# Optimization experiments

Measured on AMD Instinct MI355X. Metric: run time of the kernel, lower is better.

## Reference

```python
import jax, jax.numpy as jnp
import numpy as np

B_SZ, L_SEQ = 8, 4096
D_MODEL, D_CONV, D_MAMBA = 512, 256, 256
DSTATE, N_HEADS, K, FFN = 64, 4, 3, 2048
EPS = 1e-6


def setup_inputs() -> dict:
    key = jax.random.key(0)
    ks = jax.random.split(key, 14)
    def rn(k, shape, scale=0.02):
        return jax.random.normal(k, shape, jnp.float32) * scale
    return {
        "x": rn(ks[0], (B_SZ, L_SEQ, D_MODEL), 1.0),
        "velocity": rn(ks[1], (B_SZ, L_SEQ, D_MODEL), 0.1),
        "pre_norm_w": jnp.ones((D_MODEL,), jnp.float32),
        "conv_in_w": rn(ks[2], (D_MODEL, 2 * D_CONV)),
        "conv_dw_w": rn(ks[3], (D_CONV, K), 0.1),
        "conv_dw_b": jnp.zeros((D_CONV,), jnp.float32),
        "x_proj_w": rn(ks[4], (D_MODEL, D_MAMBA)),
        "dt_w": rn(ks[5], (D_MODEL, D_MAMBA), 0.001),
        "dt_b": jnp.full((D_MAMBA,), -4.0, jnp.float32),
        "B_w": rn(ks[6], (D_MODEL, DSTATE)),
        "C_w": rn(ks[7], (D_MODEL, DSTATE)),
        "A_log": jnp.tile(jnp.log(jnp.arange(1, DSTATE + 1, dtype=jnp.float32))[None, :], (N_HEADS, 1)),
        "D": jnp.ones((D_MAMBA,), jnp.float32),
        "ssm_out_w": rn(ks[8], (D_MAMBA, D_MAMBA)),
        "out_proj_w": rn(ks[9], (D_MODEL, D_MODEL)),
        "log_beta": jnp.asarray(0.0, jnp.float32),  # sigmoid(0)=0.5 = beta_init
        "ffn_norm_w": jnp.ones((D_MODEL,), jnp.float32),
        "w1": rn(ks[10], (D_MODEL, FFN)),
        "w3": rn(ks[11], (D_MODEL, FFN)),
        "w2": rn(ks[12], (FFN, D_MODEL)),
    }


def _rmsnorm(x, w):
    xf = x.astype(jnp.float32)
    r = jax.lax.rsqrt(jnp.mean(xf * xf, axis=-1, keepdims=True) + EPS)
    return (xf * r).astype(x.dtype) * w


def _gated_conv(xn, conv_in_w, conv_dw_w, conv_dw_b):
    # project to 2*d_conv, causal depthwise conv on first half, silu-gate with second half
    uv = xn @ conv_in_w                       # [B,L,2*dc]
    u, g = uv[..., :D_CONV], uv[..., D_CONV:]
    up = jnp.pad(u, ((0, 0), (K - 1, 0), (0, 0)))
    L = xn.shape[1]
    conv = conv_dw_b
    for k in range(K):                        # tiny fixed kernel loop
        conv = conv + up[:, k:k + L, :] * conv_dw_w[:, k]
    return conv * jax.nn.silu(g)              # [B,L,d_conv]


def _ssm(xn, x_proj_w, dt_w, dt_b, B_w, C_w, A_log, D, ssm_out_w):
    x_ssm = xn @ x_proj_w                                     # [B,L,dm]
    dt_raw = jnp.clip(xn @ dt_w + dt_b, -10.0, 5.0)
    dt = jnp.clip(jax.nn.softplus(dt_raw), 1e-4, 0.1)         # [B,L,dm]
    Bm = xn @ B_w                                             # [B,L,ds]
    Cm = xn @ C_w
    Bm = Bm / jnp.clip(jnp.linalg.norm(Bm, axis=-1, keepdims=True), 1.0)
    Cm = Cm / jnp.clip(jnp.linalg.norm(Cm, axis=-1, keepdims=True), 1.0)
    A = -jnp.exp(A_log.reshape(-1))                           # [dm], channel c -> head c//ds, state c%ds
    Bfull = jnp.tile(Bm, (1, 1, N_HEADS))                     # [B,L,dm]: B[..., c % ds]
    Cfull = jnp.tile(Cm, (1, 1, N_HEADS))
    decay = jnp.exp(dt * A)                                   # [B,L,dm]
    inp = dt * Bfull * x_ssm

    def step(h, di):
        d_, i_ = di
        h = d_ * h + i_
        return h, h

    h0 = jnp.zeros((xn.shape[0], D_MAMBA), x_ssm.dtype)
    _, hs = jax.lax.scan(step, h0, (jnp.swapaxes(decay, 0, 1), jnp.swapaxes(inp, 0, 1)))
    y = jnp.swapaxes(hs, 0, 1) * Cfull + D * x_ssm            # [B,L,dm]
    return y @ ssm_out_w


def reference(x, velocity, pre_norm_w, conv_in_w, conv_dw_w, conv_dw_b,
              x_proj_w, dt_w, dt_b, B_w, C_w, A_log, D, ssm_out_w,
              out_proj_w, log_beta, ffn_norm_w, w1, w3, w2):
    xn = _rmsnorm(x, pre_norm_w)
    conv_out = _gated_conv(xn, conv_in_w, conv_dw_w, conv_dw_b)
    ssm_out = _ssm(xn, x_proj_w, dt_w, dt_b, B_w, C_w, A_log, D, ssm_out_w)
    mixer = jnp.concatenate([conv_out, ssm_out], axis=-1) @ out_proj_w
    beta = jax.nn.sigmoid(log_beta)
    velocity = beta * velocity + mixer
    x = x + velocity
    # fused manual RMSNorm (fp32) + SwiGLU + residual
    xf = x.astype(jnp.float32)
    rms = jax.lax.rsqrt(jnp.mean(xf * xf, axis=-1, keepdims=True) + EPS)
    normed = (xf * rms).astype(x.dtype) * ffn_norm_w
    ffn = (jax.nn.silu(normed @ w1) * (normed @ w3)) @ w2
    x = x + ffn
    return (x, velocity)
```

## Files before the change

kernel.cpp:

```cpp
#include <hip/hip_runtime.h>

#define MTOK   32768
#define LSEQ   4096
#define BSZ    8
#define DM     512
#define DC     256
#define DMAMBA 256
#define DST    64
#define NPROJ  1152
#define FFN_D  2048
#define NCH    64
#define CLEN   64

typedef __attribute__((ext_vector_type(4))) float          f32x4;
typedef __attribute__((ext_vector_type(8))) unsigned short u16x8;
typedef __attribute__((ext_vector_type(8))) __bf16         bf16x8;

typedef const __attribute__((address_space(1))) unsigned int* gptr_t;
typedef __attribute__((address_space(3))) unsigned int*       lptr_t;

static __device__ __forceinline__ unsigned short f2bf(float f) {
    unsigned int u = __builtin_bit_cast(unsigned int, f);
    u += 0x7fffu + ((u >> 16) & 1u);
    return (unsigned short)(u >> 16);
}

static __device__ __forceinline__ float wred(float s) {
#pragma unroll
    for (int m = 1; m < 64; m <<= 1) s += __shfl_xor(s, m);
    return s;
}

static __device__ __forceinline__ f32x4 mfma16(u16x8 a, u16x8 b, f32x4 c) {
    return __builtin_amdgcn_mfma_f32_16x16x32_bf16(
        __builtin_bit_cast(bf16x8, a), __builtin_bit_cast(bf16x8, b), c, 0, 0, 0);
}

static __device__ __forceinline__ void gl16(const unsigned short* g, unsigned short* l) {
    __builtin_amdgcn_global_load_lds((gptr_t)g, (lptr_t)l, 16, 0, 0);
}

template <int EPI>
__global__ __launch_bounds__(256) void gemm_nt(
    const unsigned short* __restrict__ A, const unsigned short* __restrict__ Bt,
    const unsigned short* __restrict__ B2t, void* __restrict__ Cp,
    const float* __restrict__ Cin, int K, int ldc)
{
    __shared__ unsigned short As[128 * 32];
    __shared__ unsigned short Bs[128 * 32];
    __shared__ unsigned short Bs2[(EPI == 2) ? 128 * 32 : 8];

    const int tid = threadIdx.x;
    const int lane = tid & 63, wid = tid >> 6;
    const int wr = wid >> 1, wc = wid & 1;
    const long n0 = (long)blockIdx.x * 128;
    const long m0 = (long)blockIdx.y * 128;

    f32x4 acc[4][4], acc2[4][4];
#pragma unroll
    for (int i = 0; i < 4; i++)
#pragma unroll
        for (int j = 0; j < 4; j++) {
            acc[i][j] = f32x4{0.f, 0.f, 0.f, 0.f};
            acc2[i][j] = f32x4{0.f, 0.f, 0.f, 0.f};
        }

    const int srow = wid * 32 + (lane >> 2);
    const int scol = (lane & 3) * 8;
    const unsigned short* agp = A + (m0 + srow) * (long)K + scol;
    const unsigned short* bgp = Bt + (n0 + srow) * (long)K + scol;
    const unsigned short* b2gp = (EPI == 2) ? (B2t + (n0 + srow) * (long)K + scol) : nullptr;
    unsigned short* lA = As + wid * 1024;
    unsigned short* lB = Bs + wid * 1024;
    unsigned short* lB2 = (EPI == 2) ? (Bs2 + wid * 1024) : nullptr;

    const int fr = lane & 15, fo = (lane >> 4) * 8;
    const long skip = 16 * (long)K;

    for (int k0 = 0; k0 < K; k0 += 32) {
        gl16(agp + k0, lA);
        gl16(agp + k0 + skip, lA + 512);
        gl16(bgp + k0, lB);
        gl16(bgp + k0 + skip, lB + 512);
        if constexpr (EPI == 2) {
            gl16(b2gp + k0, lB2);
            gl16(b2gp + k0 + skip, lB2 + 512);
        }
        __syncthreads();

        u16x8 av[4], bv[4], cv[4];
#pragma unroll
        for (int i = 0; i < 4; i++)
            av[i] = *(const u16x8*)(As + (wr * 64 + i * 16 + fr) * 32 + fo);
#pragma unroll
        for (int j = 0; j < 4; j++)
            bv[j] = *(const u16x8*)(Bs + (wc * 64 + j * 16 + fr) * 32 + fo);
        if constexpr (EPI == 2) {
#pragma unroll
            for (int j = 0; j < 4; j++)
                cv[j] = *(const u16x8*)(Bs2 + (wc * 64 + j * 16 + fr) * 32 + fo);
        }
#pragma unroll
        for (int i = 0; i < 4; i++)
#pragma unroll
            for (int j = 0; j < 4; j++) {
                acc[i][j] = mfma16(av[i], bv[j], acc[i][j]);
                if constexpr (EPI == 2) acc2[i][j] = mfma16(av[i], cv[j], acc2[i][j]);
            }
        __syncthreads();
    }

    const int frow = (lane >> 4) * 4;
#pragma unroll
    for (int i = 0; i < 4; i++)
#pragma unroll
        for (int j = 0; j < 4; j++)
#pragma unroll
            for (int r = 0; r < 4; r++) {
                long row = m0 + wr * 64 + i * 16 + frow + r;
                long col = n0 + wc * 64 + j * 16 + fr;
                long idx = row * (long)ldc + col;
                float v = acc[i][j][r];
                if constexpr (EPI == 0) {
                    ((float*)Cp)[idx] = v;
                } else if constexpr (EPI == 1) {
                    ((unsigned short*)Cp)[idx] = f2bf(v);
                } else if constexpr (EPI == 2) {
                    float h3 = acc2[i][j][r];
                    float s = v / (1.f + __expf(-v));
                    ((unsigned short*)Cp)[idx] = f2bf(s * h3);
                } else {
                    ((float*)Cp)[idx] = Cin[idx] + v;
                }
            }
}

struct TD { const float* s; unsigned short* d; int K, N, nb; };
struct TP { TD t[10]; };

__global__ __launch_bounds__(256) void transpose_all_k(TP p)
{
    int b = blockIdx.x;
#pragma unroll
    for (int i = 0; i < 10; i++) {
        TD td = p.t[i];
        if (b < td.nb) {
            int idx = b * 256 + threadIdx.x;
            if (idx < td.K * td.N) {
                int k = idx / td.N, n = idx - k * td.N;
                td.d[(long)n * td.K + k] = f2bf(td.s[idx]);
            }
            return;
        }
        b -= td.nb;
    }
}

__global__ __launch_bounds__(256) void rmsnorm1_k(const float* __restrict__ x,
                                                  const float* __restrict__ w,
                                                  unsigned short* __restrict__ out)
{
    const int lane = threadIdx.x & 63, wv = threadIdx.x >> 6;
    const long tok = (long)blockIdx.x * 4 + wv;
    const float* xr = x + tok * DM;
    float4 v[2];
    float s = 0.f;
#pragma unroll
    for (int j = 0; j < 2; j++) {
        int d0 = j * 256 + lane * 4;
        v[j] = *(const float4*)(xr + d0);
        s += v[j].x * v[j].x + v[j].y * v[j].y + v[j].z * v[j].z + v[j].w * v[j].w;
    }
    s = wred(s);
    float r = rsqrtf(s * (1.f / DM) + 1e-6f);
#pragma unroll
    for (int j = 0; j < 2; j++) {
        int d0 = j * 256 + lane * 4;
        const float4 ww = *(const float4*)(w + d0);
        *(ushort4*)(out + tok * DM + d0) = make_ushort4(
            f2bf(v[j].x * r * ww.x), f2bf(v[j].y * r * ww.y),
            f2bf(v[j].z * r * ww.z), f2bf(v[j].w * r * ww.w));
    }
}

__global__ __launch_bounds__(256) void mamba_prep_k(
    const float* __restrict__ proj, const float* __restrict__ dt_b,
    const float* __restrict__ A_log, const float* __restrict__ conv_w,
    const float* __restrict__ conv_b,
    float* __restrict__ decay, float* __restrict__ inp, float* __restrict__ cmn,
    unsigned short* __restrict__ mixin)
{
    const int lane = threadIdx.x & 63, wv = threadIdx.x >> 6;
    const long tok = (long)blockIdx.x * 4 + wv;
    const int l = (int)(tok & (LSEQ - 1));
    const float* pr = proj + tok * NPROJ;

    float bv = pr[1024 + lane];
    float cv = pr[1088 + lane];
    float nb2 = wred(bv * bv);
    float nc2 = wred(cv * cv);
    float rb = 1.f / fmaxf(sqrtf(nb2), 1.f);
    float rc = 1.f / fmaxf(sqrtf(nc2), 1.f);
    float bn = bv * rb;
    cmn[tok * DST + lane] = cv * rc;

#pragma unroll
    for (int j = 0; j < 4; j++) {
        int d = j * 64 + lane;
        float dtr = pr[768 + d] + dt_b[d];
        dtr = fminf(fmaxf(dtr, -10.f), 5.f);
        float sp = log1pf(__expf(dtr));
        float dt = fminf(fmaxf(sp, 1e-4f), 0.1f);
        float a = -__expf(A_log[d]);
        decay[tok * DMAMBA + d] = __expf(dt * a);
        inp[tok * DMAMBA + d] = dt * bn * pr[512 + d];

        float ul  = pr[d];
        float um1 = (l >= 1) ? pr[d - NPROJ] : 0.f;
        float um2 = (l >= 2) ? pr[d - 2 * NPROJ] : 0.f;
        float conv = conv_b[d] + um2 * conv_w[d * 3] + um1 * conv_w[d * 3 + 1] + ul * conv_w[d * 3 + 2];
        float g = pr[256 + d];
        float sg = g / (1.f + __expf(-g));
        mixin[tok * DM + d] = f2bf(conv * sg);
    }
}

__global__ __launch_bounds__(256) void scan_chunk_k(const float* __restrict__ decay,
                                                    const float* __restrict__ inp,
                                                    float* __restrict__ P, float* __restrict__ S)
{
    const int bc = blockIdx.x;
    const int b = bc >> 6, c = bc & 63;
    const int d = threadIdx.x;
    long base = ((long)b * LSEQ + (long)c * CLEN) * DMAMBA + d;
    float h = 0.f, p = 1.f;
    for (int t = 0; t < CLEN; t++) {
        float dec = decay[base + (long)t * DMAMBA];
        float iv = inp[base + (long)t * DMAMBA];
        h = dec * h + iv;
        p *= dec;
    }
    P[(long)bc * DMAMBA + d] = p;
    S[(long)bc * DMAMBA + d] = h;
}

__global__ __launch_bounds__(256) void scan_prefix_k(const float* __restrict__ P,
                                                     const float* __restrict__ S,
                                                     float* __restrict__ carry)
{
    const int b = blockIdx.x, d = threadIdx.x;
    float H = 0.f;
    for (int c = 0; c < NCH; c++) {
        long i = ((long)b * NCH + c) * DMAMBA + d;
        carry[i] = H;
        H = P[i] * H + S[i];
    }
}

__global__ __launch_bounds__(256) void scan_finish_k(
    const float* __restrict__ decay, const float* __restrict__ inp,
    const float* __restrict__ carry, const float* __restrict__ cmn,
    const float* __restrict__ Dw, const float* __restrict__ proj,
    unsigned short* __restrict__ y)
{
    const int bc = blockIdx.x;
    const int b = bc >> 6, c = bc & 63;
    const int d = threadIdx.x;
    const long tok0 = (long)b * LSEQ + (long)c * CLEN;
    float h = carry[(long)bc * DMAMBA + d];
    const float dv = Dw[d];
    for (int t = 0; t < CLEN; t++) {
        long tok = tok0 + t;
        long idx = tok * DMAMBA + d;
        h = decay[idx] * h + inp[idx];
        float yv = h * cmn[tok * DST + (d & 63)] + dv * proj[tok * NPROJ + 512 + d];
        y[idx] = f2bf(yv);
    }
}

__global__ __launch_bounds__(256) void update_norm_k(
    const float* __restrict__ x, const float* __restrict__ vel,
    const float* __restrict__ mixer, const float* __restrict__ lbeta,
    const float* __restrict__ fw, float* __restrict__ outX,
    float* __restrict__ outV, unsigned short* __restrict__ normed)
{
    const int lane = threadIdx.x & 63, wv = threadIdx.x >> 6;
    const long tok = (long)blockIdx.x * 4 + wv;
    const float beta = 1.f / (1.f + __expf(-lbeta[0]));
    float xs[8];
    float s = 0.f;
#pragma unroll
    for (int j = 0; j < 2; j++) {
        const int d0 = j * 256 + lane * 4;
        const float4 xv = *(const float4*)(x + tok * DM + d0);
        const float4 vv = *(const float4*)(vel + tok * DM + d0);
        const float4 mv = *(const float4*)(mixer + tok * DM + d0);
        float4 vn, xn;
        vn.x = beta * vv.x + mv.x; xn.x = xv.x + vn.x;
        vn.y = beta * vv.y + mv.y; xn.y = xv.y + vn.y;
        vn.z = beta * vv.z + mv.z; xn.z = xv.z + vn.z;
        vn.w = beta * vv.w + mv.w; xn.w = xv.w + vn.w;
        *(float4*)(outV + tok * DM + d0) = vn;
        *(float4*)(outX + tok * DM + d0) = xn;
        s += xn.x * xn.x + xn.y * xn.y + xn.z * xn.z + xn.w * xn.w;
        xs[j * 4 + 0] = xn.x; xs[j * 4 + 1] = xn.y; xs[j * 4 + 2] = xn.z; xs[j * 4 + 3] = xn.w;
    }
    s = wred(s);
    const float r = rsqrtf(s * (1.f / DM) + 1e-6f);
#pragma unroll
    for (int j = 0; j < 2; j++) {
        const int d0 = j * 256 + lane * 4;
        const float4 ww = *(const float4*)(fw + d0);
        *(ushort4*)(normed + tok * DM + d0) = make_ushort4(
            f2bf(xs[j * 4 + 0] * r * ww.x), f2bf(xs[j * 4 + 1] * r * ww.y),
            f2bf(xs[j * 4 + 2] * r * ww.z), f2bf(xs[j * 4 + 3] * r * ww.w));
    }
}

extern "C" void kernel_launch(void* const* d_in, const int* in_sizes, int n_in,
                              void* d_out, int out_size, void* d_ws, size_t ws_size,
                              hipStream_t stream)
{
    (void)in_sizes; (void)n_in; (void)out_size; (void)ws_size;

    const float* x          = (const float*)d_in[0];
    const float* velocity   = (const float*)d_in[1];
    const float* pre_norm_w = (const float*)d_in[2];
    const float* conv_in_w  = (const float*)d_in[3];
    const float* conv_dw_w  = (const float*)d_in[4];
    const float* conv_dw_b  = (const float*)d_in[5];
    const float* x_proj_w   = (const float*)d_in[6];
    const float* dt_w       = (const float*)d_in[7];
    const float* dt_b       = (const float*)d_in[8];
    const float* B_w        = (const float*)d_in[9];
    const float* C_w        = (const float*)d_in[10];
    const float* A_log      = (const float*)d_in[11];
    const float* Dw         = (const float*)d_in[12];
    const float* ssm_out_w  = (const float*)d_in[13];
    const float* out_proj_w = (const float*)d_in[14];
    const float* log_beta   = (const float*)d_in[15];
    const float* ffn_norm_w = (const float*)d_in[16];
    const float* w1         = (const float*)d_in[17];
    const float* w3         = (const float*)d_in[18];
    const float* w2         = (const float*)d_in[19];

    char* base = (char*)d_ws;
    size_t off = 0;
    auto take = [&](size_t bytes) -> void* {
        void* p = base + off;
        off = (off + bytes + 255) & ~(size_t)255;
        return p;
    };
    unsigned short* WCAT  = (unsigned short*)take((size_t)NPROJ * DM * 2);
    unsigned short* SSMT  = (unsigned short*)take((size_t)DMAMBA * DMAMBA * 2);
    unsigned short* OUTPT = (unsigned short*)take((size_t)DM * DM * 2);
    unsigned short* W1T   = (unsigned short*)take((size_t)FFN_D * DM * 2);
    unsigned short* W3T   = (unsigned short*)take((size_t)FFN_D * DM * 2);
    unsigned short* W2T   = (unsigned short*)take((size_t)DM * FFN_D * 2);
    unsigned short* XN    = (unsigned short*)take((size_t)MTOK * DM * 2);
    float* PROJ  = (float*)take((size_t)MTOK * NPROJ * 4);
    float* DECAY = (float*)take((size_t)MTOK * DMAMBA * 4);
    float* INP   = (float*)take((size_t)MTOK * DMAMBA * 4);
    float* CMN   = (float*)take((size_t)MTOK * DST * 4);
    float* PP    = (float*)take((size_t)BSZ * NCH * DMAMBA * 4);
    float* SS    = (float*)take((size_t)BSZ * NCH * DMAMBA * 4);
    float* CARRY = (float*)take((size_t)BSZ * NCH * DMAMBA * 4);
    unsigned short* Y      = (unsigned short*)take((size_t)MTOK * DMAMBA * 2);
    unsigned short* MIXIN  = (unsigned short*)take((size_t)MTOK * DM * 2);
    unsigned short* NORMED = (unsigned short*)take((size_t)MTOK * DM * 2);
    float* MIXER = DECAY;
    unsigned short* ACT = XN;
    float* outX = (float*)d_out;
    float* outV = outX + (size_t)MTOK * DM;

    TP tp;
    int tblk = 0;
    auto addT = [&](int i, const float* s, unsigned short* dst, int K, int N) {
        int nb = (K * N + 255) / 256;
        tp.t[i] = TD{s, dst, K, N, nb};
        tblk += nb;
    };
    addT(0, conv_in_w, WCAT, DM, DM);
    addT(1, x_proj_w, WCAT + 512 * DM, DM, DMAMBA);
    addT(2, dt_w, WCAT + 768 * DM, DM, DMAMBA);
    addT(3, B_w, WCAT + 1024 * DM, DM, DST);
    addT(4, C_w, WCAT + 1088 * DM, DM, DST);
    addT(5, ssm_out_w, SSMT, DMAMBA, DMAMBA);
    addT(6, out_proj_w, OUTPT, DM, DM);
    addT(7, w1, W1T, DM, FFN_D);
    addT(8, w3, W3T, DM, FFN_D);
    addT(9, w2, W2T, FFN_D, DM);
    transpose_all_k<<<tblk, 256, 0, stream>>>(tp);

    rmsnorm1_k<<<MTOK / 4, 256, 0, stream>>>(x, pre_norm_w, XN);

    gemm_nt<0><<<dim3(NPROJ / 128, MTOK / 128), 256, 0, stream>>>(
        XN, WCAT, nullptr, PROJ, nullptr, DM, NPROJ);

    mamba_prep_k<<<MTOK / 4, 256, 0, stream>>>(PROJ, dt_b, A_log, conv_dw_w, conv_dw_b,
                                               DECAY, INP, CMN, MIXIN);

    scan_chunk_k<<<BSZ * NCH, 256, 0, stream>>>(DECAY, INP, PP, SS);
    scan_prefix_k<<<BSZ, 256, 0, stream>>>(PP, SS, CARRY);
    scan_finish_k<<<BSZ * NCH, 256, 0, stream>>>(DECAY, INP, CARRY, CMN, Dw, PROJ, Y);

    gemm_nt<1><<<dim3(DMAMBA / 128, MTOK / 128), 256, 0, stream>>>(
        Y, SSMT, nullptr, (void*)(MIXIN + 256), nullptr, DMAMBA, DM);

    gemm_nt<0><<<dim3(DM / 128, MTOK / 128), 256, 0, stream>>>(
        MIXIN, OUTPT, nullptr, MIXER, nullptr, DM, DM);

    update_norm_k<<<MTOK / 4, 256, 0, stream>>>(x, velocity, MIXER, log_beta, ffn_norm_w,
                                                outX, outV, NORMED);

    gemm_nt<2><<<dim3(FFN_D / 128, MTOK / 128), 256, 0, stream>>>(
        NORMED, W1T, W3T, ACT, nullptr, DM, FFN_D);

    gemm_nt<3><<<dim3(DM / 128, MTOK / 128), 256, 0, stream>>>(
        ACT, W2T, nullptr, (void*)outX, (const float*)outX, FFN_D, DM);
}
```

Before: 1.002 ms.

## Double-buffer LDS tiles in GEMM to overlap global loads with MFMA

The GEMM main loop now keeps two LDS buffers and issues the global-to-LDS loads for the next K slice before computing on the current one. A single barrier per iteration replaces the previous pair of barriers. The aim is to hide global load latency behind MFMA work, at the cost of twice the shared memory, which can lower occupancy, especially for the dual-B SwiGLU variant.

```diff
diff --git a/kernel.cpp b/kernel.cpp
--- a/kernel.cpp
+++ b/kernel.cpp
@@ -46,9 +46,9 @@
     const unsigned short* __restrict__ B2t, void* __restrict__ Cp,
     const float* __restrict__ Cin, int K, int ldc)
 {
-    __shared__ unsigned short As[128 * 32];
-    __shared__ unsigned short Bs[128 * 32];
-    __shared__ unsigned short Bs2[(EPI == 2) ? 128 * 32 : 8];
+    __shared__ unsigned short As[2 * 128 * 32];
+    __shared__ unsigned short Bs[2 * 128 * 32];
+    __shared__ unsigned short Bs2[(EPI == 2) ? 2 * 128 * 32 : 8];
 
     const int tid = threadIdx.x;
     const int lane = tid & 63, wid = tid >> 6;
@@ -70,35 +70,39 @@
     const unsigned short* agp = A + (m0 + srow) * (long)K + scol;
     const unsigned short* bgp = Bt + (n0 + srow) * (long)K + scol;
     const unsigned short* b2gp = (EPI == 2) ? (B2t + (n0 + srow) * (long)K + scol) : nullptr;
-    unsigned short* lA = As + wid * 1024;
-    unsigned short* lB = Bs + wid * 1024;
-    unsigned short* lB2 = (EPI == 2) ? (Bs2 + wid * 1024) : nullptr;
+    const long skip = 16 * (long)K;
 
     const int fr = lane & 15, fo = (lane >> 4) * 8;
-    const long skip = 16 * (long)K;
-
-    for (int k0 = 0; k0 < K; k0 += 32) {
-        gl16(agp + k0, lA);
-        gl16(agp + k0 + skip, lA + 512);
-        gl16(bgp + k0, lB);
-        gl16(bgp + k0 + skip, lB + 512);
+
+    auto STAGE = [&](int buf, int k0) {
+        unsigned short* dA = As + buf * 4096 + wid * 1024;
+        unsigned short* dB = Bs + buf * 4096 + wid * 1024;
+        gl16(agp + k0, dA);
+        gl16(agp + k0 + skip, dA + 512);
+        gl16(bgp + k0, dB);
+        gl16(bgp + k0 + skip, dB + 512);
         if constexpr (EPI == 2) {
-            gl16(b2gp + k0, lB2);
-            gl16(b2gp + k0 + skip, lB2 + 512);
+            unsigned short* dB2 = Bs2 + buf * 4096 + wid * 1024;
+            gl16(b2gp + k0, dB2);
+            gl16(b2gp + k0 + skip, dB2 + 512);
         }
-        __syncthreads();
-
+    };
+
+    auto COMPUTE = [&](int buf) {
+        const unsigned short* sA = As + buf * 4096;
+        const unsigned short* sB = Bs + buf * 4096;
         u16x8 av[4], bv[4], cv[4];
 #pragma unroll
         for (int i = 0; i < 4; i++)
-            av[i] = *(const u16x8*)(As + (wr * 64 + i * 16 + fr) * 32 + fo);
+            av[i] = *(const u16x8*)(sA + (wr * 64 + i * 16 + fr) * 32 + fo);
 #pragma unroll
         for (int j = 0; j < 4; j++)
-            bv[j] = *(const u16x8*)(Bs + (wc * 64 + j * 16 + fr) * 32 + fo);
+            bv[j] = *(const u16x8*)(sB + (wc * 64 + j * 16 + fr) * 32 + fo);
         if constexpr (EPI == 2) {
+            const unsigned short* sB2 = Bs2 + buf * 4096;
 #pragma unroll
             for (int j = 0; j < 4; j++)
-                cv[j] = *(const u16x8*)(Bs2 + (wc * 64 + j * 16 + fr) * 32 + fo);
+                cv[j] = *(const u16x8*)(sB2 + (wc * 64 + j * 16 + fr) * 32 + fo);
         }
 #pragma unroll
         for (int i = 0; i < 4; i++)
@@ -107,8 +111,18 @@
                 acc[i][j] = mfma16(av[i], bv[j], acc[i][j]);
                 if constexpr (EPI == 2) acc2[i][j] = mfma16(av[i], cv[j], acc2[i][j]);
             }
+    };
+
+    STAGE(0, 0);
+    __syncthreads();
+    int cur = 0;
+    for (int k0 = 32; k0 < K; k0 += 32) {
+        STAGE(cur ^ 1, k0);
+        COMPUTE(cur);
         __syncthreads();
-    }
+        cur ^= 1;
+    }
+    COMPUTE(cur);
 
     const int frow = (lane >> 4) * 4;
 #pragma unroll
```

Result: faster. 883.6 us (-11.8%).
